# Kernel tuning notes

Measured on AMD Instinct MI355X. Metric: run time of the kernel, lower is better.

## Reference

```python
import jax, jax.numpy as jnp
import numpy as np

VOCAB = 50257
D = 128           # vector_dim
S = 128           # sentence_length
B = 4096


def setup_inputs() -> dict:
    key = jax.random.key(0)
    ks = jax.random.split(key, 10)
    x = jax.random.randint(ks[0], (B, S), 0, VOCAB)
    target_char = jax.random.randint(ks[1], (B, 1), 0, VOCAB)
    emb = jax.random.normal(ks[2], (VOCAB, D), dtype=jnp.float32) * 0.02
    emb = emb.at[0].set(0.0)  # padding_idx=0
    tgt_emb = jax.random.normal(ks[3], (VOCAB, D), dtype=jnp.float32) * 0.02
    s = 1.0 / np.sqrt(D)
    W_ih = jax.random.uniform(ks[4], (2 * D, D), jnp.float32, -s, s)  # input->hidden (transposed)
    W_hh = jax.random.uniform(ks[5], (D, D), jnp.float32, -s, s)
    b_ih = jax.random.uniform(ks[6], (D,), jnp.float32, -s, s)
    b_hh = jax.random.uniform(ks[7], (D,), jnp.float32, -s, s)
    W_cls = jax.random.uniform(ks[8], (D, S), jnp.float32, -s, s)    # Linear(d, sentence_length), transposed
    b_cls = jax.random.uniform(ks[9], (S,), jnp.float32, -s, s)
    return {"x": x, "target_char": target_char, "emb": emb, "tgt_emb": tgt_emb,
            "W_ih": W_ih, "W_hh": W_hh, "b_ih": b_ih, "b_hh": b_hh,
            "W_cls": W_cls, "b_cls": b_cls}


def reference(x, target_char, emb, tgt_emb, W_ih, W_hh, b_ih, b_hh, W_cls, b_cls):
    seq_embed = emb[x]                                   # [B, S, D]
    target_embed = tgt_emb[target_char[:, 0]]            # [B, D]
    target_bcast = jnp.broadcast_to(target_embed[:, None, :], (seq_embed.shape[0], S, D))
    combined = jnp.concatenate([seq_embed, target_bcast], axis=2)  # [B, S, 2D]

    # vanilla tanh RNN: h_t = tanh(x_t @ W_ih + b_ih + h_{t-1} @ W_hh + b_hh)
    xs = jnp.transpose(combined, (1, 0, 2))              # [S, B, 2D]
    h0 = jnp.zeros((combined.shape[0], D), dtype=combined.dtype)

    def step(h, x_t):
        h_new = jnp.tanh(x_t @ W_ih + b_ih + h @ W_hh + b_hh)
        return h_new, None

    h_last, _ = jax.lax.scan(step, h0, xs)               # [B, D]
    logits = h_last @ W_cls + b_cls                      # [B, S]
    return jax.nn.softmax(logits, axis=-1)
```

## Files before the change

kernel.cpp:

```cpp
#include <hip/hip_runtime.h>

#define VOCAB 50257
#define NGRP  3142
#define SCL   2048.0f
#define ISCL  (1.0f / 2048.0f)

typedef _Float16 half8 __attribute__((ext_vector_type(8)));
typedef _Float16 half4 __attribute__((ext_vector_type(4)));
typedef float    f32x4 __attribute__((ext_vector_type(4)));

__device__ __forceinline__ float fast_tanh(float x) {
    float e = __expf(2.0f * x);
    float r = __builtin_amdgcn_rcpf(e + 1.0f);
    return fmaf(-2.0f, r, 1.0f);
}
__device__ __forceinline__ void splitf(float v, _Float16& hi, _Float16& lo) {
    hi = (_Float16)v;
    lo = (_Float16)((v - (float)hi) * SCL);
}

__device__ __forceinline__ void load_w4(const float* __restrict__ W,
        int ncol, int g, half8 (&wHi)[4], half8 (&wLo)[4])
{
#pragma unroll
    for (int kc = 0; kc < 4; ++kc) {
        const int kb = kc * 32 + g * 8;
        half8 hv, lv;
#pragma unroll
        for (int i = 0; i < 8; ++i) {
            float w = W[(size_t)(kb + i) * 128 + ncol];
            _Float16 hi, lo; splitf(w, hi, lo);
            hv[i] = hi; lv[i] = lo;
        }
        wHi[kc] = hv; wLo[kc] = lv;
    }
}

__device__ __forceinline__ void mfma3(half8 aH, half8 aL, half8 bH, half8 bL,
                                      f32x4& accA, f32x4& accB)
{
    accA = __builtin_amdgcn_mfma_f32_16x16x32_f16(aH, bH, accA, 0, 0, 0);
    accB = __builtin_amdgcn_mfma_f32_16x16x32_f16(aH, bL, accB, 0, 0, 0);
    accB = __builtin_amdgcn_mfma_f32_16x16x32_f16(aL, bH, accB, 0, 0, 0);
}

__global__ __launch_bounds__(256) void emb_proj_mfma(
    const float* __restrict__ emb, const float* __restrict__ W_ih,
    float* __restrict__ emb_proj)
{
    __shared__ __align__(16) float bounce[16 * 132];
    const int t = threadIdx.x;
    const int w = t >> 6, lane = t & 63, g = lane >> 4, ln = lane & 15;

    half8 wHi[2][4], wLo[2][4];
    load_w4(W_ih, 32 * w + ln,      g, wHi[0], wLo[0]);
    load_w4(W_ih, 32 * w + 16 + ln, g, wHi[1], wLo[1]);

    for (int grp = blockIdx.x; grp < NGRP; grp += gridDim.x) {
        const int vb = grp * 16;
        int arow = vb + ln; if (arow >= VOCAB) arow = VOCAB - 1;
        const float* rp = emb + (size_t)arow * 128 + g * 8;
        half8 aHi[4], aLo[4];
#pragma unroll
        for (int kc = 0; kc < 4; ++kc) {
            float4 v0 = *(const float4*)(rp + kc * 32);
            float4 v1 = *(const float4*)(rp + kc * 32 + 4);
            float vv[8] = {v0.x, v0.y, v0.z, v0.w, v1.x, v1.y, v1.z, v1.w};
            half8 hv, lv;
#pragma unroll
            for (int i = 0; i < 8; ++i) {
                _Float16 hi, lo; splitf(vv[i], hi, lo);
                hv[i] = hi; lv[i] = lo;
            }
            aHi[kc] = hv; aLo[kc] = lv;
        }
        f32x4 accA[2], accB[2];
#pragma unroll
        for (int nt = 0; nt < 2; ++nt) {
            accA[nt] = {0.f, 0.f, 0.f, 0.f};
            accB[nt] = {0.f, 0.f, 0.f, 0.f};
        }
#pragma unroll
        for (int nt = 0; nt < 2; ++nt)
#pragma unroll
            for (int kc = 0; kc < 4; ++kc)
                mfma3(aHi[kc], aLo[kc], wHi[nt][kc], wLo[nt][kc],
                      accA[nt], accB[nt]);

        __syncthreads();
#pragma unroll
        for (int nt = 0; nt < 2; ++nt) {
            const int n = 32 * w + 16 * nt + ln;
#pragma unroll
            for (int r = 0; r < 4; ++r)
                bounce[(4 * g + r) * 132 + n] =
                    accA[nt][r] + accB[nt][r] * ISCL;
        }
        __syncthreads();
        const int r2 = t >> 4, c8 = (t & 15) * 8;
        const int vrow = vb + r2;
        if (vrow < VOCAB) {
            float4 o0 = *(const float4*)&bounce[r2 * 132 + c8];
            float4 o1 = *(const float4*)&bounce[r2 * 132 + c8 + 4];
            *(float4*)&emb_proj[(size_t)vrow * 128 + c8]     = o0;
            *(float4*)&emb_proj[(size_t)vrow * 128 + c8 + 4] = o1;
        }
    }
}

__global__ __launch_bounds__(512) void rnn_mfma(
    const int* __restrict__ x, const int* __restrict__ tc,
    const float* __restrict__ tgt_emb,
    const float* __restrict__ W_ih, const float* __restrict__ W_hh,
    const float* __restrict__ b_ih, const float* __restrict__ b_hh,
    const float* __restrict__ W_cls, const float* __restrict__ b_cls,
    const float* __restrict__ ep, float* __restrict__ out)
{
    __shared__ _Float16 sHi[2][16 * 128];
    __shared__ _Float16 sLo[2][16 * 128];
    __shared__ int   xs[16 * 132];
    __shared__ float red[2][8][16];

    const int t = threadIdx.x;
    const int w = t >> 6, lane = t & 63, g = lane >> 4, ln = lane & 15;
    const int rb0 = blockIdx.x * 16;
    const int j0  = w * 16 + 4 * g;

    for (int i = t; i < 16 * 132; i += 512) {
        int b = i / 132, s = i - b * 132;
        xs[i] = (s < 128) ? x[(size_t)(rb0 + b) * 128 + s] : 0;
    }
    {
        const int b = t >> 5, k0 = (t & 31) * 4;
        const int tok = tc[rb0 + b];
        float4 v = *(const float4*)(tgt_emb + (size_t)tok * 128 + k0);
        float vv[4] = {v.x, v.y, v.z, v.w};
        half4 hv, lv;
#pragma unroll
        for (int i = 0; i < 4; ++i) {
            _Float16 hi, lo; splitf(vv[i], hi, lo);
            hv[i] = hi; lv[i] = lo;
        }
        const int a = b * 128 + (((k0 >> 3) ^ (b & 7)) << 3) + (k0 & 7);
        *(half4*)&sHi[0][a] = hv;
        *(half4*)&sLo[0][a] = lv;
    }
    __syncthreads();

    half8 wHi[4], wLo[4];
    load_w4(W_ih + 128 * 128, w * 16 + ln, g, wHi, wLo);
    f32x4 cc;
    {
        half8 bH[4], bL[4];
#pragma unroll
        for (int kc = 0; kc < 4; ++kc) {
            const int a = ln * 128 + (((kc * 4 + g) ^ (ln & 7)) << 3);
            bH[kc] = *(const half8*)&sHi[0][a];
            bL[kc] = *(const half8*)&sLo[0][a];
        }
        float4 bi = *(const float4*)&b_ih[j0];
        float4 bh = *(const float4*)&b_hh[j0];
        f32x4 cA = {bi.x + bh.x, bi.y + bh.y, bi.z + bh.z, bi.w + bh.w};
        f32x4 cB = {0.f, 0.f, 0.f, 0.f};
#pragma unroll
        for (int kc = 0; kc < 4; ++kc)
            mfma3(wHi[kc], wLo[kc], bH[kc], bL[kc], cA, cB);
        cc = cA + cB * ISCL;
    }
    __syncthreads();
    for (int i = t; i < 16 * 128; i += 512) {
        sHi[0][i] = (_Float16)0.f;
        sLo[0][i] = (_Float16)0.f;
    }

    load_w4(W_hh, w * 16 + ln, g, wHi, wLo);

    int4 tk = *(const int4*)&xs[ln * 132];
    f32x4 uc;
    {
        unsigned uo = ((unsigned)tk.x << 7) + (unsigned)j0;
        float4 v = *(const float4*)(ep + uo);
        uc[0] = v.x; uc[1] = v.y; uc[2] = v.z; uc[3] = v.w;
    }
    __syncthreads();

#define RSTEP(CUR, NXT, TOKN) do {                                          \
    unsigned uo_ = ((unsigned)(TOKN) << 7) + (unsigned)j0;                  \
    float4 vn_ = *(const float4*)(ep + uo_);                                \
    half8 bH_[4], bL_[4];                                                   \
    _Pragma("unroll")                                                       \
    for (int kc = 0; kc < 4; ++kc) {                                        \
        const int a_ = ln * 128 + (((kc * 4 + g) ^ (ln & 7)) << 3);         \
        bH_[kc] = *(const half8*)&sHi[CUR][a_];                             \
        bL_[kc] = *(const half8*)&sLo[CUR][a_];                             \
    }                                                                       \
    f32x4 accA_ = cc + uc;                                                  \
    f32x4 accB_ = {0.f, 0.f, 0.f, 0.f};                                     \
    _Pragma("unroll")                                                       \
    for (int kc = 0; kc < 4; ++kc)                                          \
        mfma3(wHi[kc], wLo[kc], bH_[kc], bL_[kc], accA_, accB_);            \
    half4 hv_, lv_;                                                         \
    _Pragma("unroll")                                                       \
    for (int r = 0; r < 4; ++r) {                                           \
        float th_ = fast_tanh(accA_[r] + accB_[r] * ISCL);                  \
        _Float16 hi_, lo_; splitf(th_, hi_, lo_);                           \
        hv_[r] = hi_; lv_[r] = lo_;                                         \
    }                                                                       \
    {                                                                       \
        const int a_ = ln * 128 + (((j0 >> 3) ^ (ln & 7)) << 3) + (j0 & 7); \
        *(half4*)&sHi[NXT][a_] = hv_;                                       \
        *(half4*)&sLo[NXT][a_] = lv_;                                       \
    }                                                                       \
    __syncthreads();                                                        \
    uc[0] = vn_.x; uc[1] = vn_.y; uc[2] = vn_.z; uc[3] = vn_.w;             \
} while (0)

    for (int sb = 0; sb < 32; ++sb) {
        int4 tkn = *(const int4*)&xs[ln * 132 + 4 * (sb + 1)];
        RSTEP(0, 1, tk.y);
        RSTEP(1, 0, tk.z);
        RSTEP(0, 1, tk.w);
        RSTEP(1, 0, tkn.x);
        tk = tkn;
    }
#undef RSTEP

    load_w4(W_cls, w * 16 + ln, g, wHi, wLo);
    f32x4 L;
    {
        half8 bH[4], bL[4];
#pragma unroll
        for (int kc = 0; kc < 4; ++kc) {
            const int a = ln * 128 + (((kc * 4 + g) ^ (ln & 7)) << 3);
            bH[kc] = *(const half8*)&sHi[0][a];
            bL[kc] = *(const half8*)&sLo[0][a];
        }
        float4 bc = *(const float4*)&b_cls[j0];
        f32x4 lA = {bc.x, bc.y, bc.z, bc.w};
        f32x4 lB = {0.f, 0.f, 0.f, 0.f};
#pragma unroll
        for (int kc = 0; kc < 4; ++kc)
            mfma3(wHi[kc], wLo[kc], bH[kc], bL[kc], lA, lB);
        L = lA + lB * ISCL;
    }

    float mx = fmaxf(fmaxf(L[0], L[1]), fmaxf(L[2], L[3]));
    mx = fmaxf(mx, __shfl_xor(mx, 16, 64));
    mx = fmaxf(mx, __shfl_xor(mx, 32, 64));
    if (lane < 16) red[0][w][ln] = mx;
    __syncthreads();
    float gm = red[0][0][ln];
#pragma unroll
    for (int ww = 1; ww < 8; ++ww) gm = fmaxf(gm, red[0][ww][ln]);
    float sum = 0.f;
#pragma unroll
    for (int r = 0; r < 4; ++r) { L[r] = __expf(L[r] - gm); sum += L[r]; }
    sum += __shfl_xor(sum, 16, 64);
    sum += __shfl_xor(sum, 32, 64);
    if (lane < 16) red[1][w][ln] = sum;
    __syncthreads();
    float tot = 0.f;
#pragma unroll
    for (int ww = 0; ww < 8; ++ww) tot += red[1][ww][ln];
    const float inv = 1.0f / tot;
#pragma unroll
    for (int r = 0; r < 4; ++r)
        out[(size_t)(rb0 + ln) * 128 + j0 + r] = L[r] * inv;
}

extern "C" void kernel_launch(void* const* d_in, const int* in_sizes, int n_in,
                              void* d_out, int out_size, void* d_ws, size_t ws_size,
                              hipStream_t stream)
{
    const int*   x     = (const int*)d_in[0];
    const int*   tc    = (const int*)d_in[1];
    const float* emb   = (const float*)d_in[2];
    const float* tgt   = (const float*)d_in[3];
    const float* W_ih  = (const float*)d_in[4];
    const float* W_hh  = (const float*)d_in[5];
    const float* b_ih  = (const float*)d_in[6];
    const float* b_hh  = (const float*)d_in[7];
    const float* W_cls = (const float*)d_in[8];
    const float* b_cls = (const float*)d_in[9];
    float* out = (float*)d_out;
    float* emb_proj = (float*)d_ws;

    emb_proj_mfma<<<1024, 256, 0, stream>>>(emb, W_ih, emb_proj);
    rnn_mfma<<<256, 512, 0, stream>>>(x, tc, tgt, W_ih, W_hh,
                                      b_ih, b_hh, W_cls, b_cls,
                                      emb_proj, out);
}
```

Baseline: 225.0 us.

## Split MFMA correction accumulators, prefetch two steps ahead, use lightweight LDS barrier

Each correction MFMA now writes to its own accumulator, so the three MFMAs per k-chunk form three independent chains and the back-to-back dependency on one accumulator goes away. The recurrent loop loads the projected embedding row two timesteps ahead instead of one, which hides more of the global-load latency. The per-step __syncthreads is replaced with an inline s_waitcnt lgkmcnt(0) plus s_barrier, so the barrier no longer waits on outstanding global prefetch loads. In exchange it uses extra registers and depends on hand-written barrier semantics being correct.

```diff
diff --git a/kernel.cpp b/kernel.cpp
--- a/kernel.cpp
+++ b/kernel.cpp
@@ -9,6 +9,8 @@
 typedef _Float16 half4 __attribute__((ext_vector_type(4)));
 typedef float    f32x4 __attribute__((ext_vector_type(4)));
 
+#define LDS_BAR() asm volatile("s_waitcnt lgkmcnt(0)\n\ts_barrier" ::: "memory")
+
 __device__ __forceinline__ float fast_tanh(float x) {
     float e = __expf(2.0f * x);
     float r = __builtin_amdgcn_rcpf(e + 1.0f);
@@ -36,12 +38,12 @@
     }
 }
 
-__device__ __forceinline__ void mfma3(half8 aH, half8 aL, half8 bH, half8 bL,
-                                      f32x4& accA, f32x4& accB)
+__device__ __forceinline__ void mfma3s(half8 aH, half8 aL, half8 bH, half8 bL,
+                                       f32x4& accA, f32x4& accB, f32x4& accC)
 {
     accA = __builtin_amdgcn_mfma_f32_16x16x32_f16(aH, bH, accA, 0, 0, 0);
     accB = __builtin_amdgcn_mfma_f32_16x16x32_f16(aH, bL, accB, 0, 0, 0);
-    accB = __builtin_amdgcn_mfma_f32_16x16x32_f16(aL, bH, accB, 0, 0, 0);
+    accC = __builtin_amdgcn_mfma_f32_16x16x32_f16(aL, bH, accC, 0, 0, 0);
 }
 
 __global__ __launch_bounds__(256) void emb_proj_mfma(
@@ -74,18 +76,19 @@
             }
             aHi[kc] = hv; aLo[kc] = lv;
         }
-        f32x4 accA[2], accB[2];
+        f32x4 accA[2], accB[2], accC[2];
 #pragma unroll
         for (int nt = 0; nt < 2; ++nt) {
             accA[nt] = {0.f, 0.f, 0.f, 0.f};
             accB[nt] = {0.f, 0.f, 0.f, 0.f};
+            accC[nt] = {0.f, 0.f, 0.f, 0.f};
         }
 #pragma unroll
         for (int nt = 0; nt < 2; ++nt)
 #pragma unroll
             for (int kc = 0; kc < 4; ++kc)
-                mfma3(aHi[kc], aLo[kc], wHi[nt][kc], wLo[nt][kc],
-                      accA[nt], accB[nt]);
+                mfma3s(aHi[kc], aLo[kc], wHi[nt][kc], wLo[nt][kc],
+                       accA[nt], accB[nt], accC[nt]);
 
         __syncthreads();
 #pragma unroll
@@ -94,7 +97,7 @@
 #pragma unroll
             for (int r = 0; r < 4; ++r)
                 bounce[(4 * g + r) * 132 + n] =
-                    accA[nt][r] + accB[nt][r] * ISCL;
+                    accA[nt][r] + (accB[nt][r] + accC[nt][r]) * ISCL;
         }
         __syncthreads();
         const int r2 = t >> 4, c8 = (t & 15) * 8;
@@ -162,10 +165,11 @@
         float4 bh = *(const float4*)&b_hh[j0];
         f32x4 cA = {bi.x + bh.x, bi.y + bh.y, bi.z + bh.z, bi.w + bh.w};
         f32x4 cB = {0.f, 0.f, 0.f, 0.f};
+        f32x4 cC = {0.f, 0.f, 0.f, 0.f};
 #pragma unroll
         for (int kc = 0; kc < 4; ++kc)
-            mfma3(wHi[kc], wLo[kc], bH[kc], bL[kc], cA, cB);
-        cc = cA + cB * ISCL;
+            mfma3s(wHi[kc], wLo[kc], bH[kc], bL[kc], cA, cB, cC);
+        cc = cA + (cB + cC) * ISCL;
     }
     __syncthreads();
     for (int i = t; i < 16 * 128; i += 512) {
@@ -176,17 +180,20 @@
     load_w4(W_hh, w * 16 + ln, g, wHi, wLo);
 
     int4 tk = *(const int4*)&xs[ln * 132];
-    f32x4 uc;
+    f32x4 uc0, uc1;
     {
-        unsigned uo = ((unsigned)tk.x << 7) + (unsigned)j0;
-        float4 v = *(const float4*)(ep + uo);
-        uc[0] = v.x; uc[1] = v.y; uc[2] = v.z; uc[3] = v.w;
-    }
-    __syncthreads();
-
-#define RSTEP(CUR, NXT, TOKN) do {                                          \
-    unsigned uo_ = ((unsigned)(TOKN) << 7) + (unsigned)j0;                  \
-    float4 vn_ = *(const float4*)(ep + uo_);                                \
+        unsigned a0 = ((unsigned)tk.x << 7) + (unsigned)j0;
+        unsigned a1 = ((unsigned)tk.y << 7) + (unsigned)j0;
+        float4 v0 = *(const float4*)(ep + a0);
+        float4 v1 = *(const float4*)(ep + a1);
+        uc0[0] = v0.x; uc0[1] = v0.y; uc0[2] = v0.z; uc0[3] = v0.w;
+        uc1[0] = v1.x; uc1[1] = v1.y; uc1[2] = v1.z; uc1[3] = v1.w;
+    }
+    __syncthreads();
+
+#define RSTEP(CUR, NXT, TOK2) do {                                          \
+    unsigned uo_ = ((unsigned)(TOK2) << 7) + (unsigned)j0;                  \
+    float4 v2_ = *(const float4*)(ep + uo_);             \
     half8 bH_[4], bL_[4];                                                   \
     _Pragma("unroll")                                                       \
     for (int kc = 0; kc < 4; ++kc) {                                        \
@@ -194,15 +201,16 @@
         bH_[kc] = *(const half8*)&sHi[CUR][a_];                             \
         bL_[kc] = *(const half8*)&sLo[CUR][a_];                             \
     }                                                                       \
-    f32x4 accA_ = cc + uc;                                                  \
+    f32x4 accA_ = cc + uc0;                                                 \
     f32x4 accB_ = {0.f, 0.f, 0.f, 0.f};                                     \
+    f32x4 accC_ = {0.f, 0.f, 0.f, 0.f};                                     \
     _Pragma("unroll")                                                       \
     for (int kc = 0; kc < 4; ++kc)                                          \
-        mfma3(wHi[kc], wLo[kc], bH_[kc], bL_[kc], accA_, accB_);            \
+        mfma3s(wHi[kc], wLo[kc], bH_[kc], bL_[kc], accA_, accB_, accC_);    \
     half4 hv_, lv_;                                                         \
     _Pragma("unroll")                                                       \
     for (int r = 0; r < 4; ++r) {                                           \
-        float th_ = fast_tanh(accA_[r] + accB_[r] * ISCL);                  \
+        float th_ = fast_tanh(accA_[r] + (accB_[r] + accC_[r]) * ISCL);     \
         _Float16 hi_, lo_; splitf(th_, hi_, lo_);                           \
         hv_[r] = hi_; lv_[r] = lo_;                                         \
     }                                                                       \
@@ -211,16 +219,17 @@
         *(half4*)&sHi[NXT][a_] = hv_;                                       \
         *(half4*)&sLo[NXT][a_] = lv_;                                       \
     }                                                                       \
-    __syncthreads();                                                        \
-    uc[0] = vn_.x; uc[1] = vn_.y; uc[2] = vn_.z; uc[3] = vn_.w;             \
+    LDS_BAR();                                                              \
+    uc0 = uc1;                                                              \
+    uc1[0] = v2_.x; uc1[1] = v2_.y; uc1[2] = v2_.z; uc1[3] = v2_.w;         \
 } while (0)
 
     for (int sb = 0; sb < 32; ++sb) {
         int4 tkn = *(const int4*)&xs[ln * 132 + 4 * (sb + 1)];
-        RSTEP(0, 1, tk.y);
-        RSTEP(1, 0, tk.z);
-        RSTEP(0, 1, tk.w);
-        RSTEP(1, 0, tkn.x);
+        RSTEP(0, 1, tk.z);
+        RSTEP(1, 0, tk.w);
+        RSTEP(0, 1, tkn.x);
+        RSTEP(1, 0, tkn.y);
         tk = tkn;
     }
 #undef RSTEP
@@ -238,10 +247,11 @@
         float4 bc = *(const float4*)&b_cls[j0];
         f32x4 lA = {bc.x, bc.y, bc.z, bc.w};
         f32x4 lB = {0.f, 0.f, 0.f, 0.f};
+        f32x4 lC = {0.f, 0.f, 0.f, 0.f};
 #pragma unroll
         for (int kc = 0; kc < 4; ++kc)
-            mfma3(wHi[kc], wLo[kc], bH[kc], bL[kc], lA, lB);
-        L = lA + lB * ISCL;
+            mfma3s(wHi[kc], wLo[kc], bH[kc], bL[kc], lA, lB, lC);
+        L = lA + (lB + lC) * ISCL;
     }
 
     float mx = fmaxf(fmaxf(L[0], L[1]), fmaxf(L[2], L[3]));
```

Measured after the change: 191.9 us. 14.7% less time.
